# Performance work log

Measured on AMD Instinct MI355X. Metric: run time of the kernel, lower is better.

Reference implementation:

```python
import jax, jax.numpy as jnp
import numpy as np

N = 100000
E = 1600000
IN_DIM = 128
H = 1
C = 64  # out_dim


def setup_inputs() -> dict:
    key = jax.random.key(0)
    k1, k2, k3, k4, k5, k6, k7 = jax.random.split(key, 7)
    x = jax.random.normal(k1, (N, IN_DIM), dtype=jnp.float32)
    edge_index = jax.random.randint(k2, (2, E), 0, N, dtype=jnp.int64)
    beta = jax.random.uniform(k3, (E,), dtype=jnp.float32)
    lam01 = jax.random.uniform(k4, (1,), dtype=jnp.float32)
    # learned params (xavier-normal-ish scale)
    W = jax.random.normal(k5, (IN_DIM, C), dtype=jnp.float32) * (1.414 * np.sqrt(2.0 / (IN_DIM + C)))
    att_src = jax.random.normal(k6, (1, H, C), dtype=jnp.float32) * (1.414 * np.sqrt(2.0 / (1 + C)))
    att_dst = jax.random.normal(k7, (1, H, C), dtype=jnp.float32) * (1.414 * np.sqrt(2.0 / (1 + C)))
    return {"x": x, "edge_index": edge_index, "beta": beta, "lam01": lam01,
            "W": W, "att_src": att_src, "att_dst": att_dst}


def _segment_softmax(e, seg, num_segments):
    # numerically stable softmax of e (E,H) grouped by seg (E,)
    m = jax.ops.segment_max(e, seg, num_segments=num_segments)
    ex = jnp.exp(e - m[seg])
    denom = jax.ops.segment_sum(ex, seg, num_segments=num_segments)
    return ex / (denom[seg] + 1e-16)


def reference(x, edge_index, beta, lam01, W, att_src, att_dst):
    n = x.shape[0]
    xp = (x @ W).reshape(n, H, C)              # (N,H,C), shared src/dst projection
    a_src = (xp * att_src).sum(-1)             # (N,H)
    a_dst = (xp * att_dst).sum(-1)             # (N,H)
    src, dst = edge_index[0], edge_index[1]
    e = jax.nn.sigmoid(a_src[src] + a_dst[dst])          # (E,H)
    alpha = _segment_softmax(e, dst, n)                   # (E,H)
    beta_h = beta[:, None]                                # (E,1) -> broadcast over H
    lam = lam01[0]
    gamma = lam * alpha + (1.0 - lam) * beta_h            # (E,H)
    msg = xp[src] * gamma[..., None]                      # (E,H,C)
    out = jax.ops.segment_sum(msg, dst, num_segments=n)   # (N,H,C)
    return out.mean(axis=1)                               # concat=False -> mean over heads
```

## Files before the change

### kernel.cpp

```cpp
#include <hip/hip_runtime.h>
#include <hip/hip_bf16.h>
#include <hip/hip_fp16.h>

#define IN_DIM 128
#define C_DIM 64
#define SH    9
#define DP    512
#define CAP   10240
#define NBKT2 256

typedef __attribute__((ext_vector_type(8))) short bf16x8;
typedef __attribute__((ext_vector_type(4))) float f32x4;

__device__ __forceinline__ short f2b(float f) {
    unsigned u = __float_as_uint(f);
    unsigned r = (u + 0x7FFFu + ((u >> 16) & 1u)) >> 16;
    return (short)r;
}

__device__ __forceinline__ int2 make_rec(int s, int dl, float b) {
    unsigned b15 = (unsigned)(b * 32767.f + 0.5f) & 0x7FFFu;
    return make_int2(s, (int)(((unsigned)dl << 15) | b15));
}

__global__ __launch_bounds__(256) void k_fused(
    const float* __restrict__ x,
    const float* __restrict__ W,
    const float* __restrict__ att_src,
    const float* __restrict__ att_dst,
    unsigned short* __restrict__ xp_bf,
    float* __restrict__ s_src,
    float* __restrict__ s_dst,
    const int* __restrict__ ei_src,
    const int* __restrict__ ei_dst,
    const float* __restrict__ beta,
    int* __restrict__ gcur,
    int2* __restrict__ gbuf,
    int n, int e, int gd, int gg, int S)
{
    __shared__ char smem[23552];

    const int bid = (int)blockIdx.x;
    const int q   = bid / S;
    const bool bin_role = (bid % S == 0) && (q < gd);
    const int chunk = bin_role ? q : (bid - min(gd, q + 1));
    const int t = threadIdx.x;

    if (bin_role) {
        int2*           stag  = (int2*)smem;
        unsigned short* sbkt  = (unsigned short*)(smem + 16384);
        int*            bcnt  = (int*)(smem + 20480);
        int*            bpre  = (int*)(smem + 21504);
        int*            gbase = (int*)(smem + 22528);

        for (int i = t; i < NBKT2; i += 256) bcnt[i] = 0;
        __syncthreads();

        const int i0 = (chunk * 256 + t) * 8;
        int   sv[8], dv[8], bkt[8], lr[8];
        float bv[8];
        int   nk = 0;
        if (i0 + 7 < e) {
            int4   sa = *(const int4*)&ei_src[i0];
            int4   sb = *(const int4*)&ei_src[i0 + 4];
            int4   da = *(const int4*)&ei_dst[i0];
            int4   db = *(const int4*)&ei_dst[i0 + 4];
            float4 ba = *(const float4*)&beta[i0];
            float4 bb = *(const float4*)&beta[i0 + 4];
            sv[0]=sa.x; sv[1]=sa.y; sv[2]=sa.z; sv[3]=sa.w;
            sv[4]=sb.x; sv[5]=sb.y; sv[6]=sb.z; sv[7]=sb.w;
            dv[0]=da.x; dv[1]=da.y; dv[2]=da.z; dv[3]=da.w;
            dv[4]=db.x; dv[5]=db.y; dv[6]=db.z; dv[7]=db.w;
            bv[0]=ba.x; bv[1]=ba.y; bv[2]=ba.z; bv[3]=ba.w;
            bv[4]=bb.x; bv[5]=bb.y; bv[6]=bb.z; bv[7]=bb.w;
            nk = 8;
        } else {
            for (int k = 0; i0 + k < e && k < 8; ++k) {
                sv[k] = ei_src[i0 + k];
                dv[k] = ei_dst[i0 + k];
                bv[k] = beta[i0 + k];
                ++nk;
            }
        }
        for (int k = 0; k < nk; ++k) {
            bkt[k] = dv[k] >> SH;
            lr[k]  = atomicAdd(&bcnt[bkt[k]], 1);
        }
        __syncthreads();

        if (t < 64) {
            int c[4], s = 0;
            #pragma unroll
            for (int j = 0; j < 4; ++j) { c[j] = bcnt[4 * t + j]; s += c[j]; }
            int v = s;
            #pragma unroll
            for (int off = 1; off < 64; off <<= 1) {
                int u = __shfl_up(v, off, 64);
                if (t >= off) v += u;
            }
            int base = v - s;
            #pragma unroll
            for (int j = 0; j < 4; ++j) { bpre[4 * t + j] = base; base += c[j]; }
        }
        __syncthreads();

        if (t < NBKT2) {
            int c = bcnt[t];
            if (c > 0) gbase[t] = atomicAdd(&gcur[t], c);
        }
        __syncthreads();

        for (int k = 0; k < nk; ++k) {
            int slot = bpre[bkt[k]] + lr[k];
            stag[slot] = make_rec(sv[k], dv[k] & (DP - 1), bv[k]);
            sbkt[slot] = (unsigned short)bkt[k];
        }
        __syncthreads();

        const int total = bpre[NBKT2 - 1] + bcnt[NBKT2 - 1];
        for (int i = t; i < total; i += 256) {
            int bb = sbkt[i];
            int al = gbase[bb] + (i - bpre[bb]);
            if (al < CAP) gbuf[(size_t)bb * CAP + al] = stag[i];
        }
        return;
    }

    short (*WT)[136] = (short(*)[136])smem;
    for (int i = t; i < IN_DIM * C_DIM; i += 256) {
        int k = i >> 6, nn = i & 63;
        WT[nn][k] = f2b(W[i]);
    }
    __syncthreads();

    const int lane = t & 63;
    const int wv   = t >> 6;
    const int base = (chunk * 4 + wv) * 16;
    if (base >= n) return;

    const int m    = lane & 15;
    const int quad = lane >> 4;
    int rowA = base + m;
    if (rowA >= n) rowA = n - 1;
    const float* xr = x + (size_t)rowA * IN_DIM + quad * 8;

    f32x4 acc[4] = {{0,0,0,0},{0,0,0,0},{0,0,0,0},{0,0,0,0}};

    #pragma unroll
    for (int ks = 0; ks < 4; ++ks) {
        float4 f0 = *(const float4*)(xr + ks * 32);
        float4 f1 = *(const float4*)(xr + ks * 32 + 4);
        bf16x8 a;
        a[0] = f2b(f0.x); a[1] = f2b(f0.y); a[2] = f2b(f0.z); a[3] = f2b(f0.w);
        a[4] = f2b(f1.x); a[5] = f2b(f1.y); a[6] = f2b(f1.z); a[7] = f2b(f1.w);
        #pragma unroll
        for (int nt = 0; nt < 4; ++nt) {
            bf16x8 bb = *(const bf16x8*)&WT[nt * 16 + m][ks * 32 + quad * 8];
            acc[nt] = __builtin_amdgcn_mfma_f32_16x16x32_bf16(a, bb, acc[nt], 0, 0, 0);
        }
    }

    float asv[4], adv[4];
    #pragma unroll
    for (int nt = 0; nt < 4; ++nt) {
        asv[nt] = att_src[nt * 16 + m];
        adv[nt] = att_dst[nt * 16 + m];
    }
    #pragma unroll
    for (int qq = 0; qq < 4; ++qq) {
        float vs = 0.f, vd = 0.f;
        #pragma unroll
        for (int nt = 0; nt < 4; ++nt) {
            vs = fmaf(acc[nt][qq], asv[nt], vs);
            vd = fmaf(acc[nt][qq], adv[nt], vd);
        }
        #pragma unroll
        for (int off = 8; off > 0; off >>= 1) {
            vs += __shfl_xor(vs, off, 64);
            vd += __shfl_xor(vd, off, 64);
        }
        int r = base + quad * 4 + qq;
        if (m == 0 && r < n) { s_src[r] = vs; s_dst[r] = vd; }
    }

    #pragma unroll
    for (int nt = 0; nt < 4; ++nt)
        #pragma unroll
        for (int qq = 0; qq < 4; ++qq) {
            int r = base + quad * 4 + qq;
            if (r < n)
                xp_bf[(size_t)r * C_DIM + nt * 16 + m] = (unsigned short)f2b(acc[nt][qq]);
        }
}

__global__ __launch_bounds__(256) void k_sort(
    const int* __restrict__ gcur,
    const int2* __restrict__ gbuf,
    int2* __restrict__ gsort,
    int2* __restrict__ gmeta,
    int n)
{
    __shared__ int cnt2[DP];
    __shared__ int pre[DP + 1];
    __shared__ int fill[DP];

    const int b = (int)blockIdx.x;
    const int t = threadIdx.x;
    const int m = min(gcur[b], CAP);

    for (int i = t; i < DP; i += 256) { cnt2[i] = 0; fill[i] = 0; }
    __syncthreads();

    for (int i = t; i < m; i += 256) {
        int y = gbuf[(size_t)b * CAP + i].y;
        atomicAdd(&cnt2[(y >> 15) & (DP - 1)], 1);
    }
    __syncthreads();

    if (t < 64) {
        int c[8], s = 0;
        #pragma unroll
        for (int j = 0; j < 8; ++j) { c[j] = cnt2[8 * t + j]; s += c[j]; }
        int v = s;
        #pragma unroll
        for (int off = 1; off < 64; off <<= 1) {
            int u = __shfl_up(v, off, 64);
            if (t >= off) v += u;
        }
        int base = v - s;
        #pragma unroll
        for (int j = 0; j < 8; ++j) { pre[8 * t + j] = base; base += c[j]; }
        if (t == 63) pre[DP] = v;
    }
    __syncthreads();

    for (int i = t; i < DP; i += 256) {
        int d = (b << SH) + i;
        if (d < n) gmeta[d] = make_int2(b * CAP + pre[i], pre[i + 1] - pre[i]);
    }
    for (int i = t; i < m; i += 256) {
        int2 r = gbuf[(size_t)b * CAP + i];
        int dl = (r.y >> 15) & (DP - 1);
        int l  = atomicAdd(&fill[dl], 1);
        gsort[(size_t)b * CAP + pre[dl] + l] = r;
    }
}

__global__ __launch_bounds__(256) void k_seg(
    const int2* __restrict__ gsort,
    const int2* __restrict__ gmeta,
    const unsigned short* __restrict__ xp_bf,
    const float* __restrict__ s_src,
    const float* __restrict__ s_dst,
    const float* __restrict__ lam01,
    float* __restrict__ out,
    int n)
{
    const int lane = threadIdx.x & 63;
    const int wv   = threadIdx.x >> 6;
    const int d0   = ((int)blockIdx.x * 4 + wv) * 2;
    if (d0 >= n) return;
    const int d1   = d0 + 1;
    const bool has1 = (d1 < n);

    const int4 mt = *(const int4*)&gmeta[d0];
    const int T0 = min(mt.y, 64);
    const int T1 = has1 ? min(mt.w, 64) : 0;
    const int Tm = max(T0, T1);

    const int half = lane & 32;
    const int l31  = lane & 31;
    const int myT   = half ? T1 : T0;
    const int myoff = half ? mt.z : mt.x;
    const int myd   = half ? (has1 ? d1 : d0) : d0;

    const float sd  = s_dst[myd];
    const float lam = lam01[0];
    const float oml = 1.f - lam;
    const float ib  = 1.f / 32767.f;

    int sx0 = 0; float ee0 = 0.f, bb0 = 0.f;
    if (l31 < myT) {
        int2 r = gsort[(size_t)myoff + l31];
        sx0 = r.x;
        bb0 = (float)(r.y & 0x7FFF) * ib;
        float z = s_src[sx0] + sd;
        ee0 = __expf(1.f / (1.f + __expf(-z)));
    }
    int sx1 = 0; float ee1 = 0.f, bb1 = 0.f;
    const bool two = (Tm > 32);
    if (two && l31 + 32 < myT) {
        int2 r = gsort[(size_t)myoff + l31 + 32];
        sx1 = r.x;
        bb1 = (float)(r.y & 0x7FFF) * ib;
        float z = s_src[sx1] + sd;
        ee1 = __expf(1.f / (1.f + __expf(-z)));
    }

    float psl = ee0 + ee1;
    #pragma unroll
    for (int off = 16; off > 0; off >>= 1) psl += __shfl_xor(psl, off, 64);
    const float gl = lam / (psl + 1e-16f);
    const float g0 = fmaf(gl, ee0, oml * bb0);
    const float g1 = fmaf(gl, ee1, oml * bb1);

    const unsigned* xp32 = (const unsigned*)xp_bf;
    float ax = 0.f, ay = 0.f;

    const int r0 = min(Tm, 32);
    int j = 0;
    for (; j + 4 <= r0; j += 4) {
        int sb[4]; float gb[4]; unsigned uu[4];
        #pragma unroll
        for (int k = 0; k < 4; ++k) {
            sb[k] = __shfl(sx0, half + j + k, 64);
            gb[k] = __shfl(g0,  half + j + k, 64);
        }
        #pragma unroll
        for (int k = 0; k < 4; ++k)
            uu[k] = xp32[(size_t)sb[k] * 32 + l31];
        #pragma unroll
        for (int k = 0; k < 4; ++k) {
            ax = fmaf(__uint_as_float(uu[k] << 16),         gb[k], ax);
            ay = fmaf(__uint_as_float(uu[k] & 0xFFFF0000u), gb[k], ay);
        }
    }
    for (; j < r0; ++j) {
        int sb = __shfl(sx0, half + j, 64);
        float gb = __shfl(g0, half + j, 64);
        unsigned u = xp32[(size_t)sb * 32 + l31];
        ax = fmaf(__uint_as_float(u << 16),         gb, ax);
        ay = fmaf(__uint_as_float(u & 0xFFFF0000u), gb, ay);
    }
    if (two) {
        const int r1 = Tm - 32;
        for (int j2 = 0; j2 < r1; ++j2) {
            int sb = __shfl(sx1, half + j2, 64);
            float gb = __shfl(g1, half + j2, 64);
            unsigned u = xp32[(size_t)sb * 32 + l31];
            ax = fmaf(__uint_as_float(u << 16),         gb, ax);
            ay = fmaf(__uint_as_float(u & 0xFFFF0000u), gb, ay);
        }
    }

    const int row = d0 + (lane >> 5);
    if (row < n) {
        float2 v; v.x = ax; v.y = ay;
        *(float2*)&out[(size_t)row * C_DIM + l31 * 2] = v;
    }
}

extern "C" void kernel_launch(void* const* d_in, const int* in_sizes, int n_in,
                              void* d_out, int out_size, void* d_ws, size_t ws_size,
                              hipStream_t stream)
{
    const float* x       = (const float*)d_in[0];
    const int*   ei      = (const int*)d_in[1];
    const float* beta    = (const float*)d_in[2];
    const float* lam01   = (const float*)d_in[3];
    const float* W       = (const float*)d_in[4];
    const float* att_src = (const float*)d_in[5];
    const float* att_dst = (const float*)d_in[6];
    float*       out     = (float*)d_out;

    const int n = in_sizes[0] / IN_DIM;
    const int e = in_sizes[2];

    const int nbkt = (n + DP - 1) / DP;

    int2*           gbuf  = (int2*)d_ws;
    int2*           gsort = gbuf + (size_t)nbkt * CAP;
    unsigned short* xp_bf = (unsigned short*)(gsort + (size_t)nbkt * CAP);
    float*          s_src = (float*)(xp_bf + (size_t)n * C_DIM);
    float*          s_dst = s_src + n;
    int2*           gmeta = (int2*)(s_dst + n);
    int*            gcur  = (int*)(gmeta + n + 2);

    const int gd = (e + 2047) / 2048;
    const int gg = (n + 63) / 64;
    const int S  = (gd + gg + gd - 1) / gd;

    hipMemsetAsync(gcur, 0, NBKT2 * sizeof(int), stream);

    k_fused<<<gd + gg, 256, 0, stream>>>(x, W, att_src, att_dst, xp_bf,
                                         s_src, s_dst, ei, ei + e, beta,
                                         gcur, gbuf, n, e, gd, gg, S);
    k_sort<<<nbkt, 256, 0, stream>>>(gcur, gbuf, gsort, gmeta, n);
    k_seg <<<(n + 7) / 8, 256, 0, stream>>>(gsort, gmeta, xp_bf, s_src, s_dst,
                                            lam01, out, n);
}
```

Baseline: 193.2 us.

## Fuse bucket sort and segment reduction into one kernel with LDS staging

Result: slower. 197.8 us (+2.3%).

```diff
diff --git a/kernel.cpp b/kernel.cpp
--- a/kernel.cpp
+++ b/kernel.cpp
@@ -8,6 +8,8 @@
 #define DP    512
 #define CAP   10240
 #define NBKT2 256
+#define DPH   256
+#define CAPH  6144
 
 typedef __attribute__((ext_vector_type(8))) short bf16x8;
 typedef __attribute__((ext_vector_type(4))) float f32x4;
@@ -193,62 +195,9 @@
         }
 }
 
-__global__ __launch_bounds__(256) void k_sort(
+__global__ __launch_bounds__(512) void k_sred(
     const int* __restrict__ gcur,
     const int2* __restrict__ gbuf,
-    int2* __restrict__ gsort,
-    int2* __restrict__ gmeta,
-    int n)
-{
-    __shared__ int cnt2[DP];
-    __shared__ int pre[DP + 1];
-    __shared__ int fill[DP];
-
-    const int b = (int)blockIdx.x;
-    const int t = threadIdx.x;
-    const int m = min(gcur[b], CAP);
-
-    for (int i = t; i < DP; i += 256) { cnt2[i] = 0; fill[i] = 0; }
-    __syncthreads();
-
-    for (int i = t; i < m; i += 256) {
-        int y = gbuf[(size_t)b * CAP + i].y;
-        atomicAdd(&cnt2[(y >> 15) & (DP - 1)], 1);
-    }
-    __syncthreads();
-
-    if (t < 64) {
-        int c[8], s = 0;
-        #pragma unroll
-        for (int j = 0; j < 8; ++j) { c[j] = cnt2[8 * t + j]; s += c[j]; }
-        int v = s;
-        #pragma unroll
-        for (int off = 1; off < 64; off <<= 1) {
-            int u = __shfl_up(v, off, 64);
-            if (t >= off) v += u;
-        }
-        int base = v - s;
-        #pragma unroll
-        for (int j = 0; j < 8; ++j) { pre[8 * t + j] = base; base += c[j]; }
-        if (t == 63) pre[DP] = v;
-    }
-    __syncthreads();
-
-    for (int i = t; i < DP; i += 256) {
-        int d = (b << SH) + i;
-        if (d < n) gmeta[d] = make_int2(b * CAP + pre[i], pre[i + 1] - pre[i]);
-    }
-    for (int i = t; i < m; i += 256) {
-        int2 r = gbuf[(size_t)b * CAP + i];
-        int dl = (r.y >> 15) & (DP - 1);
-        int l  = atomicAdd(&fill[dl], 1);
-        gsort[(size_t)b * CAP + pre[dl] + l] = r;
-    }
-}
-
-__global__ __launch_bounds__(256) void k_seg(
-    const int2* __restrict__ gsort,
-    const int2* __restrict__ gmeta,
     const unsigned short* __restrict__ xp_bf,
     const float* __restrict__ s_src,
     const float* __restrict__ s_dst,
@@ -256,97 +205,164 @@
     float* __restrict__ out,
     int n)
 {
-    const int lane = threadIdx.x & 63;
-    const int wv   = threadIdx.x >> 6;
-    const int d0   = ((int)blockIdx.x * 4 + wv) * 2;
-    if (d0 >= n) return;
-    const int d1   = d0 + 1;
-    const bool has1 = (d1 < n);
-
-    const int4 mt = *(const int4*)&gmeta[d0];
-    const int T0 = min(mt.y, 64);
-    const int T1 = has1 ? min(mt.w, 64) : 0;
-    const int Tm = max(T0, T1);
-
+    __shared__ int2 stag[CAPH];
+    __shared__ int  cnt[DPH];
+    __shared__ int  pre[DPH + 1];
+    __shared__ int  fill[DPH];
+
+    const int blk = (int)blockIdx.x;
+    const int b   = blk >> 1;
+    const int h   = blk & 1;
+    const int t   = threadIdx.x;
+    const int m   = min(gcur[b], CAP);
+    const int2* reg = gbuf + (size_t)b * CAP;
+
+    for (int i = t; i < DPH; i += 512) { cnt[i] = 0; fill[i] = 0; }
+    __syncthreads();
+
+    for (int i = t; i < m; i += 512) {
+        int dl = (reg[i].y >> 15) & (DP - 1);
+        if ((dl >> 8) == h) atomicAdd(&cnt[dl & (DPH - 1)], 1);
+    }
+    __syncthreads();
+
+    if (t < 64) {
+        int c[4], s = 0;
+        #pragma unroll
+        for (int j = 0; j < 4; ++j) { c[j] = min(cnt[4 * t + j], 64); s += c[j]; }
+        int v = s;
+        #pragma unroll
+        for (int off = 1; off < 64; off <<= 1) {
+            int u = __shfl_up(v, off, 64);
+            if (t >= off) v += u;
+        }
+        int base = v - s;
+        #pragma unroll
+        for (int j = 0; j < 4; ++j) { pre[4 * t + j] = base; base += c[j]; }
+        if (t == 63) pre[DPH] = v;
+    }
+    __syncthreads();
+
+    for (int i = t; i < m; i += 512) {
+        int2 r = reg[i];
+        int dl = (r.y >> 15) & (DP - 1);
+        if ((dl >> 8) == h) {
+            int c = dl & (DPH - 1);
+            int l = atomicAdd(&fill[c], 1);
+            int lim = pre[c + 1] - pre[c];
+            int idx = pre[c] + l;
+            if (l < lim && idx < CAPH)
+                stag[idx] = make_int2(r.x, r.y & 0x7FFF);
+        }
+    }
+    __syncthreads();
+
+    const int lane = t & 63;
+    const int wv   = t >> 6;
     const int half = lane & 32;
     const int l31  = lane & 31;
-    const int myT   = half ? T1 : T0;
-    const int myoff = half ? mt.z : mt.x;
-    const int myd   = half ? (has1 ? d1 : d0) : d0;
-
-    const float sd  = s_dst[myd];
     const float lam = lam01[0];
     const float oml = 1.f - lam;
     const float ib  = 1.f / 32767.f;
-
-    int sx0 = 0; float ee0 = 0.f, bb0 = 0.f;
-    if (l31 < myT) {
-        int2 r = gsort[(size_t)myoff + l31];
-        sx0 = r.x;
-        bb0 = (float)(r.y & 0x7FFF) * ib;
-        float z = s_src[sx0] + sd;
-        ee0 = __expf(1.f / (1.f + __expf(-z)));
-    }
-    int sx1 = 0; float ee1 = 0.f, bb1 = 0.f;
-    const bool two = (Tm > 32);
-    if (two && l31 + 32 < myT) {
-        int2 r = gsort[(size_t)myoff + l31 + 32];
-        sx1 = r.x;
-        bb1 = (float)(r.y & 0x7FFF) * ib;
-        float z = s_src[sx1] + sd;
-        ee1 = __expf(1.f / (1.f + __expf(-z)));
-    }
-
-    float psl = ee0 + ee1;
-    #pragma unroll
-    for (int off = 16; off > 0; off >>= 1) psl += __shfl_xor(psl, off, 64);
-    const float gl = lam / (psl + 1e-16f);
-    const float g0 = fmaf(gl, ee0, oml * bb0);
-    const float g1 = fmaf(gl, ee1, oml * bb1);
-
     const unsigned* xp32 = (const unsigned*)xp_bf;
-    float ax = 0.f, ay = 0.f;
-
-    const int r0 = min(Tm, 32);
-    int j = 0;
-    for (; j + 4 <= r0; j += 4) {
-        int sb[4]; float gb[4]; unsigned uu[4];
-        #pragma unroll
-        for (int k = 0; k < 4; ++k) {
-            sb[k] = __shfl(sx0, half + j + k, 64);
-            gb[k] = __shfl(g0,  half + j + k, 64);
-        }
-        #pragma unroll
-        for (int k = 0; k < 4; ++k)
-            uu[k] = xp32[(size_t)sb[k] * 32 + l31];
-        #pragma unroll
-        for (int k = 0; k < 4; ++k) {
-            ax = fmaf(__uint_as_float(uu[k] << 16),         gb[k], ax);
-            ay = fmaf(__uint_as_float(uu[k] & 0xFFFF0000u), gb[k], ay);
-        }
-    }
-    for (; j < r0; ++j) {
-        int sb = __shfl(sx0, half + j, 64);
-        float gb = __shfl(g0, half + j, 64);
-        unsigned u = xp32[(size_t)sb * 32 + l31];
-        ax = fmaf(__uint_as_float(u << 16),         gb, ax);
-        ay = fmaf(__uint_as_float(u & 0xFFFF0000u), gb, ay);
-    }
-    if (two) {
-        const int r1 = Tm - 32;
-        for (int j2 = 0; j2 < r1; ++j2) {
-            int sb = __shfl(sx1, half + j2, 64);
-            float gb = __shfl(g1, half + j2, 64);
+
+    for (int lp = wv; lp < DPH / 2; lp += 8) {
+        const int dl0 = 2 * lp;
+        const int T0a = min(pre[dl0 + 1] - pre[dl0], CAPH - pre[dl0]);
+        const int T1a = min(pre[dl0 + 2] - pre[dl0 + 1], CAPH - pre[dl0 + 1]);
+        const int T0 = max(T0a, 0), T1 = max(T1a, 0);
+        const int Tm = max(T0, T1);
+        if (Tm == 0) {
+            const int d = (b << SH) + h * DPH + dl0 + (lane >> 5);
+            if (d < n) {
+                float2 z; z.x = 0.f; z.y = 0.f;
+                *(float2*)&out[(size_t)d * C_DIM + l31 * 2] = z;
+            }
+            continue;
+        }
+
+        const int myT   = half ? T1 : T0;
+        const int myoff = half ? pre[dl0 + 1] : pre[dl0];
+        const int d     = (b << SH) + h * DPH + dl0 + (half ? 1 : 0);
+        const bool act  = (d < n);
+        const float sd  = act ? s_dst[d] : 0.f;
+
+        float ee0 = 0.f, bb0 = 0.f;
+        int   sxa = 0;
+        if (l31 < myT) {
+            int2 r = stag[myoff + l31];
+            sxa = r.x;
+            bb0 = (float)(r.y & 0x7FFF) * ib;
+            float z = s_src[sxa] + sd;
+            ee0 = __expf(1.f / (1.f + __expf(-z)));
+        }
+        float ee1 = 0.f, bb1 = 0.f;
+        int   sxb = 0;
+        const bool two = (Tm > 32);
+        if (two && l31 + 32 < myT) {
+            int2 r = stag[myoff + 32 + l31];
+            sxb = r.x;
+            bb1 = (float)(r.y & 0x7FFF) * ib;
+            float z = s_src[sxb] + sd;
+            ee1 = __expf(1.f / (1.f + __expf(-z)));
+        }
+
+        float psl = ee0 + ee1;
+        #pragma unroll
+        for (int off = 16; off > 0; off >>= 1) psl += __shfl_xor(psl, off, 64);
+        const float gl = lam / (psl + 1e-16f);
+        if (l31 < myT)
+            stag[myoff + l31].y = __float_as_int(fmaf(gl, ee0, oml * bb0));
+        if (two && l31 + 32 < myT)
+            stag[myoff + 32 + l31].y = __float_as_int(fmaf(gl, ee1, oml * bb1));
+
+        float ax = 0.f, ay = 0.f;
+        const int r0 = min(Tm, 32);
+        int j = 0;
+        for (; j + 8 <= r0; j += 8) {
+            int sb[8]; float gb[8]; unsigned uu[8];
+            #pragma unroll
+            for (int k = 0; k < 8; ++k) {
+                int2 rr = stag[myoff + j + k];
+                bool vld = (j + k < myT);
+                sb[k] = vld ? rr.x : 0;
+                gb[k] = vld ? __int_as_float(rr.y) : 0.f;
+            }
+            #pragma unroll
+            for (int k = 0; k < 8; ++k)
+                uu[k] = xp32[(size_t)sb[k] * 32 + l31];
+            #pragma unroll
+            for (int k = 0; k < 8; ++k) {
+                ax = fmaf(__uint_as_float(uu[k] << 16),         gb[k], ax);
+                ay = fmaf(__uint_as_float(uu[k] & 0xFFFF0000u), gb[k], ay);
+            }
+        }
+        for (; j < r0; ++j) {
+            int2 rr = stag[myoff + j];
+            bool vld = (j < myT);
+            int   sb = vld ? rr.x : 0;
+            float gb = vld ? __int_as_float(rr.y) : 0.f;
             unsigned u = xp32[(size_t)sb * 32 + l31];
             ax = fmaf(__uint_as_float(u << 16),         gb, ax);
             ay = fmaf(__uint_as_float(u & 0xFFFF0000u), gb, ay);
         }
-    }
-
-    const int row = d0 + (lane >> 5);
-    if (row < n) {
-        float2 v; v.x = ax; v.y = ay;
-        *(float2*)&out[(size_t)row * C_DIM + l31 * 2] = v;
+        if (two) {
+            const int r1 = Tm - 32;
+            for (int j2 = 0; j2 < r1; ++j2) {
+                int2 rr = stag[myoff + 32 + j2];
+                bool vld = (32 + j2 < myT);
+                int   sb = vld ? rr.x : 0;
+                float gb = vld ? __int_as_float(rr.y) : 0.f;
+                unsigned u = xp32[(size_t)sb * 32 + l31];
+                ax = fmaf(__uint_as_float(u << 16),         gb, ax);
+                ay = fmaf(__uint_as_float(u & 0xFFFF0000u), gb, ay);
+            }
+        }
+
+        if (act) {
+            float2 v; v.x = ax; v.y = ay;
+            *(float2*)&out[(size_t)d * C_DIM + l31 * 2] = v;
+        }
     }
 }
 
@@ -369,12 +385,10 @@
     const int nbkt = (n + DP - 1) / DP;
 
     int2*           gbuf  = (int2*)d_ws;
-    int2*           gsort = gbuf + (size_t)nbkt * CAP;
-    unsigned short* xp_bf = (unsigned short*)(gsort + (size_t)nbkt * CAP);
+    unsigned short* xp_bf = (unsigned short*)(gbuf + (size_t)nbkt * CAP);
     float*          s_src = (float*)(xp_bf + (size_t)n * C_DIM);
     float*          s_dst = s_src + n;
-    int2*           gmeta = (int2*)(s_dst + n);
-    int*            gcur  = (int*)(gmeta + n + 2);
+    int*            gcur  = (int*)(s_dst + n);
 
     const int gd = (e + 2047) / 2048;
     const int gg = (n + 63) / 64;
@@ -385,7 +399,6 @@
     k_fused<<<gd + gg, 256, 0, stream>>>(x, W, att_src, att_dst, xp_bf,
                                          s_src, s_dst, ei, ei + e, beta,
                                          gcur, gbuf, n, e, gd, gg, S);
-    k_sort<<<nbkt, 256, 0, stream>>>(gcur, gbuf, gsort, gmeta, n);
-    k_seg <<<(n + 7) / 8, 256, 0, stream>>>(gsort, gmeta, xp_bf, s_src, s_dst,
-                                            lam01, out, n);
+    k_sred<<<2 * nbkt, 512, 0, stream>>>(gcur, gbuf, xp_bf, s_src, s_dst,
+                                         lam01, out, n);
 }
```
